# Kernel optimization log

Measured on AMD Instinct MI355X. Metric: run time of the kernel, lower is better.

The kernel has to match this reference:

```python
import jax, jax.numpy as jnp
import numpy as np
import math

D_MODEL = 2048
N_HEADS = 16
D_HEAD = D_MODEL // N_HEADS
D_FF = 8192
B = 2
S = 2048
LN_EPS = 1e-5


def _rope_tables(s, d_head):
    inv_freq = 1.0 / (10000.0 ** (np.arange(0, d_head, 2, dtype=np.float32) / d_head))
    t = np.arange(s, dtype=np.float32)
    freqs = np.outer(t, inv_freq)                      # [s, d_head/2]
    emb = np.concatenate([freqs, freqs], axis=-1)      # [s, d_head]
    cos = jnp.asarray(np.cos(emb))[None, None]         # [1,1,s,d_head]
    sin = jnp.asarray(np.sin(emb))[None, None]
    return cos, sin


def setup_inputs() -> dict:
    key = jax.random.key(0)
    ks = jax.random.split(key, 12)
    x = jax.random.normal(ks[0], (B, S, D_MODEL), dtype=jnp.float32)
    cos, sin = _rope_tables(S, D_HEAD)
    # additive causal mask
    mask = jnp.where(jnp.tril(jnp.ones((S, S), dtype=bool)), 0.0, -1e9).astype(jnp.float32)[None, None]
    s_in = 1.0 / math.sqrt(D_MODEL)
    s_ff = 1.0 / math.sqrt(D_FF)
    params = {
        "ln1_g": jnp.ones((D_MODEL,), jnp.float32),
        "ln1_b": jnp.zeros((D_MODEL,), jnp.float32),
        "w_qkv": jax.random.uniform(ks[1], (D_MODEL, 3 * D_MODEL), jnp.float32, -s_in, s_in),
        "b_qkv": jax.random.uniform(ks[2], (3 * D_MODEL,), jnp.float32, -s_in, s_in),
        "w_out": jax.random.uniform(ks[3], (D_MODEL, D_MODEL), jnp.float32, -s_in, s_in),
        "b_out": jax.random.uniform(ks[4], (D_MODEL,), jnp.float32, -s_in, s_in),
        "ln2_g": jnp.ones((D_MODEL,), jnp.float32),
        "ln2_b": jnp.zeros((D_MODEL,), jnp.float32),
        "w_ff1": jax.random.uniform(ks[5], (D_MODEL, D_FF), jnp.float32, -s_in, s_in),
        "b_ff1": jax.random.uniform(ks[6], (D_FF,), jnp.float32, -s_in, s_in),
        "w_ff2": jax.random.uniform(ks[7], (D_FF, D_MODEL), jnp.float32, -s_ff, s_ff),
        "b_ff2": jax.random.uniform(ks[8], (D_MODEL,), jnp.float32, -s_ff, s_ff),
    }
    return {"x": x, "cos": cos, "sin": sin, "mask": mask, **params}


def _layernorm(x, g, b):
    m = jnp.mean(x, axis=-1, keepdims=True)
    v = jnp.var(x, axis=-1, keepdims=True)
    return (x - m) * jax.lax.rsqrt(v + LN_EPS) * g + b


def _rotate_half(x):
    x1, x2 = jnp.split(x, 2, axis=-1)
    return jnp.concatenate([-x2, x1], axis=-1)


def reference(x, cos, sin, mask,
              ln1_g, ln1_b, w_qkv, b_qkv, w_out, b_out,
              ln2_g, ln2_b, w_ff1, b_ff1, w_ff2, b_ff2):
    b, s, d = x.shape
    # attention sub-block (dropout = identity, eval mode)
    xn = _layernorm(x, ln1_g, ln1_b)
    qkv = (xn @ w_qkv + b_qkv).reshape(b, s, 3, N_HEADS, D_HEAD)
    qkv = jnp.transpose(qkv, (2, 0, 3, 1, 4))           # [3,b,h,s,dh]
    q, k, v = qkv[0], qkv[1], qkv[2]
    q = q * cos + _rotate_half(q) * sin
    k = k * cos + _rotate_half(k) * sin
    scale = 1.0 / math.sqrt(D_HEAD)
    attn = jnp.einsum('bhqd,bhkd->bhqk', q, k) * scale + mask
    attn = jax.nn.softmax(attn, axis=-1)
    a_out = jnp.einsum('bhqk,bhkd->bhqd', attn, v)
    a_out = jnp.transpose(a_out, (0, 2, 1, 3)).reshape(b, s, d)
    x = x + (a_out @ w_out + b_out)
    # MLP sub-block (exact GELU, matching torch nn.GELU default)
    xn = _layernorm(x, ln2_g, ln2_b)
    h = jax.nn.gelu(xn @ w_ff1 + b_ff1, approximate=False)
    x = x + (h @ w_ff2 + b_ff2)
    return x
```

## Files before the change

### kernel.cpp

```cpp
#include <hip/hip_runtime.h>
#include <hip/hip_bf16.h>
#include <math.h>

typedef __hip_bfloat16 bf16;
using bf16x8 = __bf16 __attribute__((ext_vector_type(8)));
using f32x4  = float  __attribute__((ext_vector_type(4)));

#define D_MODEL 2048
#define S_LEN   2048
#define NB      2
#define NH      16
#define DHEAD   128
#define DFF     8192
#define M_ROWS  (NB * S_LEN)

__device__ __forceinline__ void gload_lds16(const void* g, void* l) {
    __builtin_amdgcn_global_load_lds((const __attribute__((address_space(1))) void*)g,
                                     (__attribute__((address_space(3))) void*)l, 16, 0, 0);
}

__global__ __launch_bounds__(256) void ln_kernel(const float* __restrict__ x,
                                                 const float* __restrict__ gw,
                                                 const float* __restrict__ bw,
                                                 bf16* __restrict__ out) {
    const int row = blockIdx.x;
    const float* xr = x + (size_t)row * D_MODEL;
    const int tid = threadIdx.x;
    float4 v0 = ((const float4*)xr)[tid * 2];
    float4 v1 = ((const float4*)xr)[tid * 2 + 1];
    float s = v0.x + v0.y + v0.z + v0.w + v1.x + v1.y + v1.z + v1.w;
    float q = v0.x*v0.x + v0.y*v0.y + v0.z*v0.z + v0.w*v0.w
            + v1.x*v1.x + v1.y*v1.y + v1.z*v1.z + v1.w*v1.w;
    #pragma unroll
    for (int off = 32; off; off >>= 1) {
        s += __shfl_xor(s, off);
        q += __shfl_xor(q, off);
    }
    __shared__ float red[8];
    const int wid = tid >> 6;
    if ((tid & 63) == 0) { red[wid] = s; red[4 + wid] = q; }
    __syncthreads();
    s = red[0] + red[1] + red[2] + red[3];
    q = red[4] + red[5] + red[6] + red[7];
    const float mean = s * (1.0f / D_MODEL);
    const float var  = q * (1.0f / D_MODEL) - mean * mean;
    const float inv  = rsqrtf(var + 1e-5f);
    float4 g0 = ((const float4*)gw)[tid * 2];
    float4 g1 = ((const float4*)gw)[tid * 2 + 1];
    float4 b0 = ((const float4*)bw)[tid * 2];
    float4 b1 = ((const float4*)bw)[tid * 2 + 1];
    bf16* orow = out + (size_t)row * D_MODEL + tid * 8;
    orow[0] = __float2bfloat16((v0.x - mean) * inv * g0.x + b0.x);
    orow[1] = __float2bfloat16((v0.y - mean) * inv * g0.y + b0.y);
    orow[2] = __float2bfloat16((v0.z - mean) * inv * g0.z + b0.z);
    orow[3] = __float2bfloat16((v0.w - mean) * inv * g0.w + b0.w);
    orow[4] = __float2bfloat16((v1.x - mean) * inv * g1.x + b1.x);
    orow[5] = __float2bfloat16((v1.y - mean) * inv * g1.y + b1.y);
    orow[6] = __float2bfloat16((v1.z - mean) * inv * g1.z + b1.z);
    orow[7] = __float2bfloat16((v1.w - mean) * inv * g1.w + b1.w);
}

__global__ __launch_bounds__(256) void transpose_f2b(const float* __restrict__ in,
                                                     bf16* __restrict__ out,
                                                     int R, int C) {
    __shared__ float t[32][33];
    const int c0 = blockIdx.x * 32, r0 = blockIdx.y * 32;
    const int tx = threadIdx.x & 31, ty = threadIdx.x >> 5;
    #pragma unroll
    for (int i = ty; i < 32; i += 8) t[i][tx] = in[(size_t)(r0 + i) * C + c0 + tx];
    __syncthreads();
    #pragma unroll
    for (int i = ty; i < 32; i += 8)
        out[(size_t)(c0 + i) * R + r0 + tx] = __float2bfloat16(t[tx][i]);
}

__global__ __launch_bounds__(256) void transpose_v(const bf16* __restrict__ in,
                                                   bf16* __restrict__ out) {
    const int bh = blockIdx.z;
    const bf16* ib = in + (size_t)bh * S_LEN * DHEAD;
    bf16* ob = out + (size_t)bh * DHEAD * S_LEN;
    __shared__ float t[32][33];
    const int c0 = blockIdx.x * 32;
    const int r0 = blockIdx.y * 32;
    const int tx = threadIdx.x & 31, ty = threadIdx.x >> 5;
    #pragma unroll
    for (int i = ty; i < 32; i += 8)
        t[i][tx] = __bfloat162float(ib[(size_t)(r0 + i) * DHEAD + c0 + tx]);
    __syncthreads();
    #pragma unroll
    for (int i = ty; i < 32; i += 8)
        ob[(size_t)(c0 + i) * S_LEN + r0 + tx] = __float2bfloat16(t[tx][i]);
}

__global__ __launch_bounds__(256) void rope_kernel(bf16* __restrict__ qk,
                                                   const float* __restrict__ ct,
                                                   const float* __restrict__ st) {
    const size_t idx = (size_t)blockIdx.x * 256 + threadIdx.x;
    const int dh = (int)(idx & 63);
    const size_t rrow = idx >> 6;
    const int sidx = (int)(rrow & (S_LEN - 1));
    const int which = (int)(rrow >> 16);
    const float f = (which == 0) ? 0.08838834764831845f : 1.0f;
    bf16* p = qk + rrow * DHEAD;
    const float c  = ct[sidx * DHEAD + dh];
    const float sn = st[sidx * DHEAD + dh];
    const float x1 = __bfloat162float(p[dh]);
    const float x2 = __bfloat162float(p[dh + 64]);
    p[dh]      = __float2bfloat16((x1 * c - x2 * sn) * f);
    p[dh + 64] = __float2bfloat16((x2 * c + x1 * sn) * f);
}

template <int EPI>
__global__ __launch_bounds__(256) void gemm_kernel(const bf16* __restrict__ A,
                                                   const bf16* __restrict__ Bt,
                                                   const float* __restrict__ bias,
                                                   const float* __restrict__ resid,
                                                   void* __restrict__ outp,
                                                   int M, int N, int K, int kLen) {
    __shared__ __align__(16) bf16 As[128][64];
    __shared__ __align__(16) bf16 Bs[128][64];
    const int tid  = threadIdx.x;
    const int lane = tid & 63;
    const int wid  = tid >> 6;
    const int wr = wid >> 1, wc = wid & 1;
    const int cc = lane & 15, g = lane >> 4;
    const int csw = cc & 7;

    const int nx = gridDim.x, ny = gridDim.y, nz = gridDim.z;
    int flat = blockIdx.x + nx * (blockIdx.y + ny * blockIdx.z);
    const int nwg = nx * ny * nz;
    flat = (flat & 7) * (nwg >> 3) + (flat >> 3);
    const int bx = flat % nx;
    const int t2 = flat / nx;
    const int by = t2 % ny;
    const int bz = t2 / ny;
    const int m0 = by * 128, n0 = bx * 128;
    const int kStart = bz * kLen;

    const int srow  = lane >> 3;
    const int sslot = (lane & 7) ^ (srow & 7);
    const int sb    = sslot * 16;

    f32x4 acc[4][4];
    const f32x4 zero = {0.f, 0.f, 0.f, 0.f};
    #pragma unroll
    for (int i = 0; i < 4; i++)
        #pragma unroll
        for (int j = 0; j < 4; j++) acc[i][j] = zero;

    const char* gA = (const char*)A  + ((size_t)(m0 + wid * 32 + srow) * K) * 2 + sb;
    const char* gB = (const char*)Bt + ((size_t)(n0 + wid * 32 + srow) * K) * 2 + sb;
    char* lA = (char*)&As[0][0] + wid * 4096;
    char* lB = (char*)&Bs[0][0] + wid * 4096;
    const size_t rowK2 = (size_t)K * 2;

    for (int k0 = kStart; k0 < kStart + kLen; k0 += 64) {
        #pragma unroll
        for (int c = 0; c < 4; ++c) {
            gload_lds16(gA + (size_t)k0 * 2 + (size_t)c * 8 * rowK2, lA + c * 1024);
            gload_lds16(gB + (size_t)k0 * 2 + (size_t)c * 8 * rowK2, lB + c * 1024);
        }
        __syncthreads();
        #pragma unroll
        for (int kh = 0; kh < 2; kh++) {
            const int ux = ((kh * 4 + g) ^ csw) << 4;
            bf16x8 af[4], bfm[4];
            #pragma unroll
            for (int mi = 0; mi < 4; mi++)
                af[mi]  = *(const bf16x8*)((const char*)&As[wr * 64 + mi * 16 + cc][0] + ux);
            #pragma unroll
            for (int ni = 0; ni < 4; ni++)
                bfm[ni] = *(const bf16x8*)((const char*)&Bs[wc * 64 + ni * 16 + cc][0] + ux);
            #pragma unroll
            for (int mi = 0; mi < 4; mi++)
                #pragma unroll
                for (int ni = 0; ni < 4; ni++)
                    acc[mi][ni] = __builtin_amdgcn_mfma_f32_16x16x32_bf16(af[mi], bfm[ni], acc[mi][ni], 0, 0, 0);
        }
        __syncthreads();
    }

    #pragma unroll
    for (int mi = 0; mi < 4; mi++) {
        #pragma unroll
        for (int ni = 0; ni < 4; ni++) {
            const int colb = n0 + wc * 64 + ni * 16 + cc;
            const float bcol = bias[colb];
            #pragma unroll
            for (int r = 0; r < 4; r++) {
                const int row = m0 + wr * 64 + mi * 16 + g * 4 + r;
                const float v = acc[mi][ni][r] + bcol;
                float* o = (float*)outp;
                o[(size_t)row * N + colb] = v + resid[(size_t)row * N + colb];
            }
        }
    }
}

template <int EPI>
__global__ __launch_bounds__(512, 2) void gemm256(const bf16* __restrict__ A,
                                                  const bf16* __restrict__ Bt,
                                                  const float* __restrict__ bias,
                                                  void* __restrict__ outp,
                                                  int M, int N, int K, int kLen) {
    __shared__ __align__(16) bf16 lds[2][2][2][128][64];
    const int tid  = threadIdx.x;
    const int lane = tid & 63;
    const int wid  = tid >> 6;
    const int wave_m = wid >> 2, wave_n = wid & 3;
    const int wm16 = wave_m * 16, wn16 = wave_n * 16;
    const int cc = lane & 15, g = lane >> 4;
    const int csw = cc & 7;

    const int nx = gridDim.x, ny = gridDim.y, nz = gridDim.z;
    int flat = blockIdx.x + nx * (blockIdx.y + ny * blockIdx.z);
    const int nwg = nx * ny * nz;
    flat = (flat & 7) * (nwg >> 3) + (flat >> 3);
    const int bx = flat % nx;
    const int t2 = flat / nx;
    const int by = t2 % ny;
    const int bz = t2 / ny;
    const int m0 = by * 256, n0 = bx * 256;
    const int kStart = bz * kLen;
    const int NT = kLen >> 6;

    const int srow_lo = tid >> 3;
    const int sbyte   = ((tid & 7) ^ (srow_lo & 7)) * 16;
    const size_t rowB  = (size_t)K * 2;
    const size_t halfB = rowB * 128;
    const size_t jB    = rowB * 64;
    const char* sA = (const char*)A  + (size_t)(m0 + srow_lo) * rowB + sbyte;
    const char* sB = (const char*)Bt + (size_t)(n0 + srow_lo) * rowB + sbyte;

#define STAGE(SOP, SMH, P, K0) do {                                           \
    const char* _s = (SOP ? sB : sA) + (size_t)(SMH) * halfB + (size_t)(K0) * 2; \
    char* _d = ((char*)&lds[P][SOP][SMH][0][0]) + wid * 1024;                 \
    gload_lds16(_s, _d);                                                      \
    gload_lds16(_s + jB, _d + 8192);                                          \
} while (0)

    f32x4 acc[8][4];
    const f32x4 zero = {0.f, 0.f, 0.f, 0.f};
    #pragma unroll
    for (int i = 0; i < 8; i++)
        #pragma unroll
        for (int j = 0; j < 4; j++) acc[i][j] = zero;

#define LDA(PB, MH, MI, UX) (*(const bf16x8*)((const char*)&lds[PB][0][MH][(MI) * 32 + wm16 + cc][0] + (UX)))
#define LDB(PB, NH, NI, UX) (*(const bf16x8*)((const char*)&lds[PB][1][NH][(NI) * 64 + wn16 + cc][0] + (UX)))
#define MFMA(a, b, c) __builtin_amdgcn_mfma_f32_16x16x32_bf16(a, b, c, 0, 0, 0)

#define PHASE(PB, MH, NH, DOST, SOP, SMH, VN) do {                            \
    __builtin_amdgcn_s_setprio(1);                                            \
    _Pragma("unroll")                                                         \
    for (int kk = 0; kk < 2; ++kk) {                                          \
        const int ux = ((kk * 4 + g) ^ csw) << 4;                             \
        const bf16x8 b0 = LDB(PB, NH, 0, ux);                                 \
        const bf16x8 b1 = LDB(PB, NH, 1, ux);                                 \
        const bf16x8 a0 = LDA(PB, MH, 0, ux);                                 \
        const bf16x8 a1 = LDA(PB, MH, 1, ux);                                 \
        const bf16x8 a2 = LDA(PB, MH, 2, ux);                                 \
        const bf16x8 a3 = LDA(PB, MH, 3, ux);                                 \
        acc[(MH)*4+0][(NH)*2+0] = MFMA(a0, b0, acc[(MH)*4+0][(NH)*2+0]);      \
        acc[(MH)*4+1][(NH)*2+0] = MFMA(a1, b0, acc[(MH)*4+1][(NH)*2+0]);      \
        acc[(MH)*4+2][(NH)*2+0] = MFMA(a2, b0, acc[(MH)*4+2][(NH)*2+0]);      \
        acc[(MH)*4+3][(NH)*2+0] = MFMA(a3, b0, acc[(MH)*4+3][(NH)*2+0]);      \
        acc[(MH)*4+0][(NH)*2+1] = MFMA(a0, b1, acc[(MH)*4+0][(NH)*2+1]);      \
        acc[(MH)*4+1][(NH)*2+1] = MFMA(a1, b1, acc[(MH)*4+1][(NH)*2+1]);      \
        acc[(MH)*4+2][(NH)*2+1] = MFMA(a2, b1, acc[(MH)*4+2][(NH)*2+1]);      \
        acc[(MH)*4+3][(NH)*2+1] = MFMA(a3, b1, acc[(MH)*4+3][(NH)*2+1]);      \
    }                                                                         \
    __builtin_amdgcn_s_setprio(0);                                            \
    if (DOST) STAGE(SOP, SMH, (PB) ^ 1, k0n);                                 \
    __builtin_amdgcn_sched_barrier(0);                                        \
    asm volatile("s_waitcnt vmcnt(" VN ")" ::: "memory");                     \
    __builtin_amdgcn_s_barrier();                                             \
    __builtin_amdgcn_sched_barrier(0);                                        \
} while (0)

    STAGE(0, 0, 0, kStart);
    STAGE(1, 0, 0, kStart);
    STAGE(0, 1, 0, kStart);
    STAGE(1, 1, 0, kStart);
    __builtin_amdgcn_sched_barrier(0);
    asm volatile("s_waitcnt vmcnt(4)" ::: "memory");
    __builtin_amdgcn_s_barrier();
    __builtin_amdgcn_sched_barrier(0);

    for (int t = 0; t < NT - 1; ++t) {
        const int PB = t & 1;
        const int k0n = kStart + (t + 1) * 64;
        PHASE(PB, 0, 0, true, 0, 0, "4");
        PHASE(PB, 1, 0, true, 1, 0, "4");
        PHASE(PB, 0, 1, true, 0, 1, "6");
        PHASE(PB, 1, 1, true, 1, 1, "4");
    }
    {
        const int PB = (NT - 1) & 1;
        const int k0n = 0; (void)k0n;
        PHASE(PB, 0, 0, false, 0, 0, "2");
        PHASE(PB, 1, 0, false, 1, 0, "0");
        PHASE(PB, 0, 1, false, 0, 1, "0");
        PHASE(PB, 1, 1, false, 1, 1, "0");
    }
#undef PHASE
#undef LDA
#undef LDB
#undef MFMA
#undef STAGE

    #pragma unroll
    for (int ai = 0; ai < 8; ai++) {
        const int rowb = m0 + (ai >> 2) * 128 + (ai & 3) * 32 + wm16 + g * 4;
        #pragma unroll
        for (int bj = 0; bj < 4; bj++) {
            const int colb = n0 + (bj >> 1) * 128 + (bj & 1) * 64 + wn16 + cc;
            const float bcol = (EPI == 3) ? 0.0f : bias[colb];
            #pragma unroll
            for (int r = 0; r < 4; r++) {
                const int row = rowb + r;
                const float v = acc[ai][bj][r] + bcol;
                if (EPI == 0) {
                    const int which = colb >> 11;
                    const int h     = (colb >> 7) & 15;
                    const int dh    = colb & 127;
                    const int b     = row >> 11;
                    const int sidx  = row & (S_LEN - 1);
                    bf16* o = (bf16*)outp;
                    o[((size_t)(which * 32 + b * 16 + h) * S_LEN + sidx) * DHEAD + dh] = __float2bfloat16(v);
                } else if (EPI == 2) {
                    bf16* o = (bf16*)outp;
                    const float gel = 0.5f * v * (1.0f + erff(v * 0.70710678118f));
                    o[(size_t)row * N + colb] = __float2bfloat16(gel);
                } else {
                    float* o = (float*)outp + (size_t)bz * M * N;
                    o[(size_t)row * N + colb] = v;
                }
            }
        }
    }
}

__global__ __launch_bounds__(256) void ff2_combine(const float* __restrict__ p,
                                                   const float* __restrict__ bias,
                                                   float* __restrict__ out) {
    const size_t i4 = (size_t)blockIdx.x * 256 + threadIdx.x;
    const float4 a  = ((const float4*)out)[i4];
    const float4 p0 = ((const float4*)p)[i4];
    const float4 p1 = ((const float4*)(p + (size_t)M_ROWS * D_MODEL))[i4];
    const float4 b  = ((const float4*)bias)[i4 & (D_MODEL / 4 - 1)];
    float4 r;
    r.x = a.x + p0.x + p1.x + b.x;
    r.y = a.y + p0.y + p1.y + b.y;
    r.z = a.z + p0.z + p1.z + b.z;
    r.w = a.w + p0.w + p1.w + b.w;
    ((float4*)out)[i4] = r;
}

__global__ __launch_bounds__(256) void attn_kernel(const bf16* __restrict__ q,
                                                   const bf16* __restrict__ k,
                                                   const bf16* __restrict__ vT,
                                                   bf16* __restrict__ aout) {
    int flat = blockIdx.x + gridDim.x * blockIdx.y;
    const int nwg = gridDim.x * gridDim.y;
    flat = (flat & 7) * (nwg >> 3) + (flat >> 3);
    const int qt = (int)(gridDim.x - 1 - (flat % gridDim.x));
    const int bh = flat / gridDim.x;
    const int tid = threadIdx.x;
    const int lane = tid & 63, wid = tid >> 6;
    const int cc = lane & 15, g = lane >> 4;
    const int csw = cc & 7;
    const int q0 = qt * 64;
    const int q0w = q0 + wid * 16;
    const bf16* qb = q  + (size_t)bh * S_LEN * DHEAD;
    const char* kb2 = (const char*)(k  + (size_t)bh * S_LEN * DHEAD);
    const char* vb2 = (const char*)(vT + (size_t)bh * DHEAD * S_LEN);

    __shared__ __align__(16) bf16 Ks[2][64][128];
    __shared__ __align__(16) bf16 Vs[2][128][64];
    __shared__ __align__(16) bf16 Ps[4][16][72];

    const int kst_row = wid * 4 + (lane >> 4);
    const int kst_sl  = (lane & 15) ^ (kst_row & 7);
    const int vst_row = wid * 8 + (lane >> 3);
    const int vst_sl  = (lane & 7) ^ (vst_row & 7);

    bf16x8 qf[4];
    #pragma unroll
    for (int kk = 0; kk < 4; kk++)
        qf[kk] = *(const bf16x8*)(qb + (size_t)(q0w + cc) * DHEAD + kk * 32 + g * 8);

    f32x4 oacc[8];
    const f32x4 zero = {0.f, 0.f, 0.f, 0.f};
    #pragma unroll
    for (int d = 0; d < 8; d++) oacc[d] = zero;
    float lsum[4] = {0.f, 0.f, 0.f, 0.f};

    {
        char* ksl = (char*)&Ks[0][0][0] + wid * 1024;
        char* vsl = (char*)&Vs[0][0][0] + wid * 1024;
        #pragma unroll
        for (int i = 0; i < 4; ++i) {
            gload_lds16(kb2 + (size_t)(kst_row + i * 16) * 256 + kst_sl * 16, ksl + i * 4096);
            gload_lds16(vb2 + (size_t)(vst_row + i * 32) * (S_LEN * 2) + vst_sl * 16, vsl + i * 4096);
        }
    }
    asm volatile("s_waitcnt vmcnt(0)" ::: "memory");
    __syncthreads();

    int cur = 0;
    for (int kt = 0; kt <= qt; ++kt) {
        const int kv0 = kt * 64;
        if (kt < qt) {
            const int nv0 = kv0 + 64;
            char* ksl = (char*)&Ks[cur ^ 1][0][0] + wid * 1024;
            char* vsl = (char*)&Vs[cur ^ 1][0][0] + wid * 1024;
            #pragma unroll
            for (int i = 0; i < 4; ++i) {
                gload_lds16(kb2 + (size_t)(nv0 + kst_row + i * 16) * 256 + kst_sl * 16, ksl + i * 4096);
                gload_lds16(vb2 + (size_t)(vst_row + i * 32) * (S_LEN * 2) + (size_t)nv0 * 2 + vst_sl * 16, vsl + i * 4096);
            }
        }

        f32x4 sacc[4];
        #pragma unroll
        for (int ni = 0; ni < 4; ni++) sacc[ni] = zero;
        __builtin_amdgcn_s_setprio(1);
        #pragma unroll
        for (int kk = 0; kk < 4; kk++) {
            const int ux = ((kk * 4 + g) ^ csw) << 4;
            #pragma unroll
            for (int ni = 0; ni < 4; ni++) {
                const bf16x8 kf = *(const bf16x8*)((const char*)&Ks[cur][ni * 16 + cc][0] + ux);
                sacc[ni] = __builtin_amdgcn_mfma_f32_16x16x32_bf16(qf[kk], kf, sacc[ni], 0, 0, 0);
            }
        }
        __builtin_amdgcn_s_setprio(0);

        #pragma unroll
        for (int r = 0; r < 4; r++) {
            const int qrow = q0w + g * 4 + r;
            float p[4];
            #pragma unroll
            for (int ni = 0; ni < 4; ni++) {
                const float sv = (kv0 + ni * 16 + cc <= qrow) ? sacc[ni][r] : -1e30f;
                p[ni] = __expf(sv);
            }
            lsum[r] += (p[0] + p[1]) + (p[2] + p[3]);
            #pragma unroll
            for (int ni = 0; ni < 4; ni++)
                Ps[wid][g * 4 + r][ni * 16 + cc] = __float2bfloat16(p[ni]);
        }

        __builtin_amdgcn_s_setprio(1);
        #pragma unroll
        for (int ks = 0; ks < 2; ks++) {
            const bf16x8 pf = *(const bf16x8*)(&Ps[wid][cc][ks * 32 + g * 8]);
            const int ux = ((ks * 4 + g) ^ csw) << 4;
            #pragma unroll
            for (int d = 0; d < 8; d++) {
                const bf16x8 vf = *(const bf16x8*)((const char*)&Vs[cur][d * 16 + cc][0] + ux);
                oacc[d] = __builtin_amdgcn_mfma_f32_16x16x32_bf16(pf, vf, oacc[d], 0, 0, 0);
            }
        }
        __builtin_amdgcn_s_setprio(0);

        asm volatile("s_waitcnt vmcnt(0)" ::: "memory");
        __syncthreads();
        cur ^= 1;
    }

    const int b = bh >> 4, h = bh & 15;
    #pragma unroll
    for (int r = 0; r < 4; r++) {
        float rs = lsum[r];
        #pragma unroll
        for (int off = 1; off < 16; off <<= 1) rs += __shfl_xor(rs, off);
        const float invl = 1.0f / rs;
        const int srow = q0w + g * 4 + r;
        bf16* orow = aout + ((size_t)(b * S_LEN + srow)) * D_MODEL + h * DHEAD;
        #pragma unroll
        for (int d = 0; d < 8; d++) orow[d * 16 + cc] = __float2bfloat16(oacc[d][r] * invl);
    }
}

extern "C" void kernel_launch(void* const* d_in, const int* in_sizes, int n_in,
                              void* d_out, int out_size, void* d_ws, size_t ws_size,
                              hipStream_t stream) {
    (void)in_sizes; (void)n_in; (void)out_size; (void)ws_size;
    const float* x      = (const float*)d_in[0];
    const float* cosb   = (const float*)d_in[1];
    const float* sinb   = (const float*)d_in[2];
    const float* ln1_g  = (const float*)d_in[4];
    const float* ln1_b  = (const float*)d_in[5];
    const float* w_qkv  = (const float*)d_in[6];
    const float* b_qkv  = (const float*)d_in[7];
    const float* w_out  = (const float*)d_in[8];
    const float* b_out  = (const float*)d_in[9];
    const float* ln2_g  = (const float*)d_in[10];
    const float* ln2_b  = (const float*)d_in[11];
    const float* w_ff1  = (const float*)d_in[12];
    const float* b_ff1  = (const float*)d_in[13];
    const float* w_ff2  = (const float*)d_in[14];
    const float* b_ff2  = (const float*)d_in[15];
    float* out = (float*)d_out;

    char* ws = (char*)d_ws;
    bf16* wT_qkv = (bf16*)(ws + 0);
    bf16* wT_out = (bf16*)(ws + 25165824);
    bf16* wT_ff1 = (bf16*)(ws + 33554432);
    bf16* wT_ff2 = (bf16*)(ws + 67108864);
    bf16* xn     = (bf16*)(ws + 100663296);
    bf16* qkv    = (bf16*)(ws + 117440512);
    bf16* aoutb  = (bf16*)(ws + 167772160);
    bf16* vTb    = (bf16*)(ws + 184549376);
    bf16* hbuf   = (bf16*)(ws + 117440512);
    float* partial = (float*)(ws + 0);
    bf16* kbuf = qkv + (size_t)32 * S_LEN * DHEAD;
    bf16* vbuf = qkv + (size_t)64 * S_LEN * DHEAD;

    transpose_f2b<<<dim3(192, 64),  256, 0, stream>>>(w_qkv, wT_qkv, 2048, 6144);
    transpose_f2b<<<dim3(64, 64),   256, 0, stream>>>(w_out, wT_out, 2048, 2048);
    transpose_f2b<<<dim3(256, 64),  256, 0, stream>>>(w_ff1, wT_ff1, 2048, 8192);
    transpose_f2b<<<dim3(64, 256),  256, 0, stream>>>(w_ff2, wT_ff2, 8192, 2048);

    ln_kernel<<<M_ROWS, 256, 0, stream>>>(x, ln1_g, ln1_b, xn);
    gemm256<0><<<dim3(24, 16), 512, 0, stream>>>(xn, wT_qkv, b_qkv, qkv, M_ROWS, 6144, 2048, 2048);
    rope_kernel<<<32768, 256, 0, stream>>>(qkv, cosb, sinb);
    transpose_v<<<dim3(4, 64, 32), 256, 0, stream>>>(vbuf, vTb);
    attn_kernel<<<dim3(32, 32), 256, 0, stream>>>(qkv, kbuf, vTb, aoutb);
    gemm_kernel<1><<<dim3(16, 32), 256, 0, stream>>>(aoutb, wT_out, b_out, x, out, M_ROWS, 2048, 2048, 2048);
    ln_kernel<<<M_ROWS, 256, 0, stream>>>(out, ln2_g, ln2_b, xn);
    gemm256<2><<<dim3(32, 16), 512, 0, stream>>>(xn, wT_ff1, b_ff1, hbuf, M_ROWS, DFF, 2048, 2048);
    gemm256<3><<<dim3(8, 16, 2), 512, 0, stream>>>(hbuf, wT_ff2, nullptr, partial, M_ROWS, 2048, 8192, 4096);
    ff2_combine<<<8192, 256, 0, stream>>>(partial, b_ff2, out);
}
```

Measured before the change: 712.7 us.

## Reuse register-held A/B fragments across GEMM quadrant phases in serpentine order

Restructures the GEMM main loop so the A and B fragments read from LDS stay in registers across the four quadrant phases. Phases now run in a serpentine order (00, 01, 11, 10), so each half-tile of A or B is read from LDS once per K step instead of twice, roughly halving LDS read traffic. The loop is also unrolled by two so the ping-pong buffer index is a compile-time constant, and some vmcnt wait values are retuned. The cost is more live vector registers, which could cut occupancy, and the new loop bounds assume an even number of K tiles.

```diff
diff --git a/kernel.cpp b/kernel.cpp
--- a/kernel.cpp
+++ b/kernel.cpp
@@ -246,36 +246,66 @@
         #pragma unroll
         for (int j = 0; j < 4; j++) acc[i][j] = zero;
 
+    bf16x8 aR[2][4], bR0[2][2], bR1[2][2];
+
 #define LDA(PB, MH, MI, UX) (*(const bf16x8*)((const char*)&lds[PB][0][MH][(MI) * 32 + wm16 + cc][0] + (UX)))
 #define LDB(PB, NH, NI, UX) (*(const bf16x8*)((const char*)&lds[PB][1][NH][(NI) * 64 + wn16 + cc][0] + (UX)))
 #define MFMA(a, b, c) __builtin_amdgcn_mfma_f32_16x16x32_bf16(a, b, c, 0, 0, 0)
 
-#define PHASE(PB, MH, NH, DOST, SOP, SMH, VN) do {                            \
-    __builtin_amdgcn_s_setprio(1);                                            \
-    _Pragma("unroll")                                                         \
-    for (int kk = 0; kk < 2; ++kk) {                                          \
-        const int ux = ((kk * 4 + g) ^ csw) << 4;                             \
-        const bf16x8 b0 = LDB(PB, NH, 0, ux);                                 \
-        const bf16x8 b1 = LDB(PB, NH, 1, ux);                                 \
-        const bf16x8 a0 = LDA(PB, MH, 0, ux);                                 \
-        const bf16x8 a1 = LDA(PB, MH, 1, ux);                                 \
-        const bf16x8 a2 = LDA(PB, MH, 2, ux);                                 \
-        const bf16x8 a3 = LDA(PB, MH, 3, ux);                                 \
-        acc[(MH)*4+0][(NH)*2+0] = MFMA(a0, b0, acc[(MH)*4+0][(NH)*2+0]);      \
-        acc[(MH)*4+1][(NH)*2+0] = MFMA(a1, b0, acc[(MH)*4+1][(NH)*2+0]);      \
-        acc[(MH)*4+2][(NH)*2+0] = MFMA(a2, b0, acc[(MH)*4+2][(NH)*2+0]);      \
-        acc[(MH)*4+3][(NH)*2+0] = MFMA(a3, b0, acc[(MH)*4+3][(NH)*2+0]);      \
-        acc[(MH)*4+0][(NH)*2+1] = MFMA(a0, b1, acc[(MH)*4+0][(NH)*2+1]);      \
-        acc[(MH)*4+1][(NH)*2+1] = MFMA(a1, b1, acc[(MH)*4+1][(NH)*2+1]);      \
-        acc[(MH)*4+2][(NH)*2+1] = MFMA(a2, b1, acc[(MH)*4+2][(NH)*2+1]);      \
-        acc[(MH)*4+3][(NH)*2+1] = MFMA(a3, b1, acc[(MH)*4+3][(NH)*2+1]);      \
-    }                                                                         \
-    __builtin_amdgcn_s_setprio(0);                                            \
-    if (DOST) STAGE(SOP, SMH, (PB) ^ 1, k0n);                                 \
+#define FENCE(DOST, SOP, SMH, PB, K0N, VN) do {                               \
+    if (DOST) STAGE(SOP, SMH, (PB) ^ 1, K0N);                                 \
     __builtin_amdgcn_sched_barrier(0);                                        \
     asm volatile("s_waitcnt vmcnt(" VN ")" ::: "memory");                     \
     __builtin_amdgcn_s_barrier();                                             \
     __builtin_amdgcn_sched_barrier(0);                                        \
+} while (0)
+
+#define MMQ(MB, NB_, AHR, BHR) do {                                           \
+    __builtin_amdgcn_s_setprio(1);                                            \
+    _Pragma("unroll")                                                         \
+    for (int kk = 0; kk < 2; ++kk)                                            \
+        _Pragma("unroll")                                                     \
+        for (int mi = 0; mi < 4; ++mi)                                        \
+            _Pragma("unroll")                                                 \
+            for (int ni = 0; ni < 2; ++ni)                                    \
+                acc[(MB) + mi][(NB_) + ni] =                                  \
+                    MFMA(AHR[kk][mi], BHR[kk][ni], acc[(MB) + mi][(NB_) + ni]); \
+    __builtin_amdgcn_s_setprio(0);                                            \
+} while (0)
+
+#define TILE(PB, DOST, K0N, V1, V2, V3, V4) do {                              \
+                        \
+    _Pragma("unroll")                                                         \
+    for (int kk = 0; kk < 2; ++kk) {                                          \
+        const int ux = ((kk * 4 + g) ^ csw) << 4;                             \
+        _Pragma("unroll")                                                     \
+        for (int mi = 0; mi < 4; ++mi) aR[kk][mi] = LDA(PB, 0, mi, ux);       \
+        _Pragma("unroll")                                                     \
+        for (int ni = 0; ni < 2; ++ni) bR0[kk][ni] = LDB(PB, 0, ni, ux);      \
+    }                                                                         \
+    MMQ(0, 0, aR, bR0);                                                       \
+    FENCE(DOST, 0, 0, PB, K0N, V1);                                           \
+                      \
+    _Pragma("unroll")                                                         \
+    for (int kk = 0; kk < 2; ++kk) {                                          \
+        const int ux = ((kk * 4 + g) ^ csw) << 4;                             \
+        _Pragma("unroll")                                                     \
+        for (int ni = 0; ni < 2; ++ni) bR1[kk][ni] = LDB(PB, 1, ni, ux);      \
+    }                                                                         \
+    MMQ(0, 2, aR, bR1);                                                       \
+    FENCE(DOST, 1, 0, PB, K0N, V2);                                           \
+                     \
+    _Pragma("unroll")                                                         \
+    for (int kk = 0; kk < 2; ++kk) {                                          \
+        const int ux = ((kk * 4 + g) ^ csw) << 4;                             \
+        _Pragma("unroll")                                                     \
+        for (int mi = 0; mi < 4; ++mi) aR[kk][mi] = LDA(PB, 1, mi, ux);       \
+    }                                                                         \
+    MMQ(4, 2, aR, bR1);                                                       \
+    FENCE(DOST, 0, 1, PB, K0N, V3);                                           \
+           \
+    MMQ(4, 0, aR, bR0);                                                       \
+    FENCE(DOST, 1, 1, PB, K0N, V4);                                           \
 } while (0)
 
     STAGE(0, 0, 0, kStart);
@@ -287,23 +317,17 @@
     __builtin_amdgcn_s_barrier();
     __builtin_amdgcn_sched_barrier(0);
 
-    for (int t = 0; t < NT - 1; ++t) {
-        const int PB = t & 1;
-        const int k0n = kStart + (t + 1) * 64;
-        PHASE(PB, 0, 0, true, 0, 0, "4");
-        PHASE(PB, 1, 0, true, 1, 0, "4");
-        PHASE(PB, 0, 1, true, 0, 1, "6");
-        PHASE(PB, 1, 1, true, 1, 1, "4");
-    }
-    {
-        const int PB = (NT - 1) & 1;
-        const int k0n = 0; (void)k0n;
-        PHASE(PB, 0, 0, false, 0, 0, "2");
-        PHASE(PB, 1, 0, false, 1, 0, "0");
-        PHASE(PB, 0, 1, false, 0, 1, "0");
-        PHASE(PB, 1, 1, false, 1, 1, "0");
-    }
-#undef PHASE
+    for (int tt = 0; tt < (NT - 2) / 2; ++tt) {
+        const int t0 = tt * 2;
+        TILE(0, true, kStart + (t0 + 1) * 64, "2", "4", "6", "4");
+        TILE(1, true, kStart + (t0 + 2) * 64, "2", "4", "6", "4");
+    }
+    TILE(0, true, kStart + (NT - 1) * 64, "2", "4", "6", "4");
+    TILE(1, false, 0, "0", "0", "0", "0");
+
+#undef TILE
+#undef MMQ
+#undef FENCE
 #undef LDA
 #undef LDB
 #undef MFMA
```

After: 672.5 us. 1.06x faster.
